# Kernel optimization log

Measured on AMD Instinct MI355X. Metric: run time of the kernel, lower is better.

## Reference

```python
import jax, jax.numpy as jnp
import numpy as np

K = 32
TEMP = 0.01
OTHERWEIGHT = 0.5
BS = 64
F = 128


def setup_inputs() -> dict:
    key = jax.random.key(0)
    k1, k2, k3 = jax.random.split(key, 3)
    feats1 = jax.random.normal(k1, (K * BS, F), dtype=jnp.float32)
    feats2 = jax.random.normal(k2, (K * BS, F), dtype=jnp.float32)
    overlap_inds = jax.random.randint(k3, (K,), 0, 2).astype(bool)
    return {"feats1": feats1, "feats2": feats2, "overlap_inds": overlap_inds, "bs": BS}


def _labels(overlap_inds, bs):
    k = overlap_inds.shape[0]
    labels1 = jnp.repeat(jnp.arange(k), bs)
    nov = (~overlap_inds).astype(jnp.int32)
    excl_nov = jnp.cumsum(nov) - nov  # exclusive count of non-overlaps before i
    class2 = jnp.where(overlap_inds, jnp.arange(k), k + excl_nov)
    labels2 = jnp.repeat(class2, bs)
    return jnp.concatenate([labels1, labels2])


def reference(feats1, feats2, overlap_inds, bs):
    n1 = feats1.shape[0]
    labels = _labels(overlap_inds, bs)            # [n]
    feats = jnp.concatenate([feats1, feats2])     # [n, F]
    n = feats.shape[0]

    logits = (feats @ feats.T) * TEMP             # [n, n]; log of exp(sim*temp)
    sim = jnp.exp(logits)

    same = labels[:, None] == labels[None, :]
    eye = jnp.eye(n, dtype=bool)
    pos_mask = same & ~eye
    neg_mask = ~same

    is2 = jnp.arange(n) >= n1                     # second-view block indicator
    cross_w = jnp.where(is2[:, None] != is2[None, :], OTHERWEIGHT, 1.0)

    neg_sum = jnp.sum(jnp.where(neg_mask, sim, 0.0), axis=1)      # [n]
    # -log(pos / neg_sum) = log(neg_sum) - logits
    per_pair_loss = cross_w * (jnp.log(neg_sum)[:, None] - logits)
    total_loss = jnp.sum(jnp.where(pos_mask, per_pair_loss, 0.0))
    total_pos = jnp.sum(pos_mask)

    # accuracy: a positive pair counts iff its sim beats ALL negatives in its row
    max_neg = jnp.max(jnp.where(neg_mask, sim, -jnp.inf), axis=1)  # [n]
    correct = pos_mask & (sim > max_neg[:, None])
    acc = jnp.sum(correct).astype(jnp.float32) / total_pos.astype(jnp.float32)

    loss = total_loss / total_pos.astype(jnp.float32)
    return acc, loss
```

## Files before the change

kernel.cpp:

```cpp
#include <hip/hip_runtime.h>
#include <math.h>

#define TEMP 0.01f

typedef __attribute__((ext_vector_type(8))) short short8;
typedef __attribute__((ext_vector_type(4))) float f32x4;
typedef __attribute__((ext_vector_type(8))) unsigned short ushort8_t;


__device__ __forceinline__ unsigned bf16_hi_bits(float x) {
  unsigned u = __float_as_uint(x);
  return (u + 0x7FFFu + ((u >> 16) & 1u)) >> 16;
}

struct HL { unsigned short h, l; };

__device__ __forceinline__ HL split1(float x) {
  unsigned hb = bf16_hi_bits(x);
  float hf = __uint_as_float(hb << 16);
  unsigned lb = bf16_hi_bits(x - hf);
  HL r;
  r.h = (unsigned short)hb;
  r.l = (unsigned short)lb;
  return r;
}

__device__ __forceinline__ void decode_ov(const int* __restrict__ ov_raw,
                                          int* s_class2, int* s_v2b,
                                          int* s_ov) {
  const int t = threadIdx.x;
  if (t < 64) {
    int v = (t < 32) ? ov_raw[t] : 0;
    bool valid = (t >= 32) || (v == 0) || (v == 1);
    unsigned long long okmask = __ballot(valid);
    bool as_int = (okmask == ~0ull);
    s_v2b[t] = 0;
    if (t < 32) {
      int o = as_int ? v : (((const unsigned char*)ov_raw)[t] ? 1 : 0);
      s_ov[t] = o;
      unsigned long long nz = __ballot((t < 32) && !o);
      int cum = __popcll(nz & ((1ull << t) - 1ull));
      int c2 = o ? t : 32 + cum;
      s_class2[t] = c2;
      s_v2b[c2] = t;
    }
  }
}

__device__ __forceinline__ int labf(int g, const int* s_class2) {
  return (g < 2048) ? (g >> 6) : s_class2[(g - 2048) >> 6];
}

__device__ __forceinline__ int slotf(int g, int cls, const int* s_v2b) {
  if (g < 2048) return g - (cls << 6);
  return ((cls < 32) ? 64 : 0) + (g - 2048 - (s_v2b[cls] << 6));
}

__global__ __launch_bounds__(256) void precompute_kernel(
    const float* __restrict__ f1, const float* __restrict__ f2,
    unsigned short* __restrict__ Ph, unsigned short* __restrict__ Pl,
    float* __restrict__ accum, int* __restrict__ counter) {
  if (blockIdx.x == 0 && threadIdx.x == 0) {
    accum[0] = 0.f; accum[1] = 0.f; accum[2] = 0.f; *counter = 0;
  }
  const int u = blockIdx.x * 256 + threadIdx.x;
  const int row = u >> 4;
  const int gid = u & 15;
  const int kc = gid >> 3, P = gid & 7;
  const int k = kc * 64 + (P ^ (row & 7)) * 8;
  const float* src = (row < 2048) ? (f1 + (size_t)row * 128)
                                  : (f2 + (size_t)(row - 2048) * 128);
  const float4 a = *(const float4*)(src + k);
  const float4 b = *(const float4*)(src + k + 4);
  ushort8_t hi, lo;
  HL s;
  s = split1(a.x); hi.s0 = s.h; lo.s0 = s.l;
  s = split1(a.y); hi.s1 = s.h; lo.s1 = s.l;
  s = split1(a.z); hi.s2 = s.h; lo.s2 = s.l;
  s = split1(a.w); hi.s3 = s.h; lo.s3 = s.l;
  s = split1(b.x); hi.s4 = s.h; lo.s4 = s.l;
  s = split1(b.y); hi.s5 = s.h; lo.s5 = s.l;
  s = split1(b.z); hi.s6 = s.h; lo.s6 = s.l;
  s = split1(b.w); hi.s7 = s.h; lo.s7 = s.l;
  *(ushort8_t*)&Ph[(size_t)row * 128 + gid * 8] = hi;
  *(ushort8_t*)&Pl[(size_t)row * 128 + gid * 8] = lo;
}

__device__ __forceinline__ void compute_tile(
    int bi, int bj, bool diag,
    const unsigned short* __restrict__ Ph, const unsigned short* __restrict__ Pl,
    unsigned short (*Ah)[64], unsigned short (*Al)[64],
    unsigned short (*Bh)[64], unsigned short (*Bl)[64],
    const int* s_class2, const int* s_v2b,
    float4* __restrict__ P4, float* __restrict__ posbuf) {
  const int ibase = bi * 128, jbase = bj * 128;
  const int t = threadIdx.x;
  const int l = t & 63;
  const int wid = t >> 6;
  const int wy = wid >> 1, wx = wid & 1;
  const int rr = l & 15;
  const int q = l >> 4;
  const int sw = l & 7;

  f32x4 acc[4][4];
#pragma unroll
  for (int mi = 0; mi < 4; ++mi)
#pragma unroll
    for (int ni = 0; ni < 4; ++ni) acc[mi][ni] = (f32x4)0.0f;

  const int gg = t & 7;
  const int r0 = t >> 3;

  for (int kc = 0; kc < 2; ++kc) {
    __syncthreads();
#pragma unroll
    for (int p = 0; p < 4; ++p) {
      const int r = r0 + 32 * p;
      const size_t arec = (size_t)(ibase + r) * 128 + kc * 64 + gg * 8;
      const ushort8_t vah = *(const ushort8_t*)&Ph[arec];
      const ushort8_t val = *(const ushort8_t*)&Pl[arec];
      *(ushort8_t*)&Ah[r][gg * 8] = vah;
      *(ushort8_t*)&Al[r][gg * 8] = val;
      if (!diag) {
        const size_t brec = (size_t)(jbase + r) * 128 + kc * 64 + gg * 8;
        const ushort8_t vbh = *(const ushort8_t*)&Ph[brec];
        const ushort8_t vbl = *(const ushort8_t*)&Pl[brec];
        *(ushort8_t*)&Bh[r][gg * 8] = vbh;
        *(ushort8_t*)&Bl[r][gg * 8] = vbl;
      }
    }
    __syncthreads();

#pragma unroll
    for (int s = 0; s < 2; ++s) {
      const int pb = ((((s << 2) | q)) ^ sw) << 3;
      short8 afh[4], afl[4], bfh[4], bfl[4];
#pragma unroll
      for (int mi = 0; mi < 4; ++mi) {
        const int ar = wy * 64 + mi * 16 + rr;
        afh[mi] = *(const short8*)&Ah[ar][pb];
        afl[mi] = *(const short8*)&Al[ar][pb];
        const int br = wx * 64 + mi * 16 + rr;
        bfh[mi] = diag ? *(const short8*)&Ah[br][pb]
                       : *(const short8*)&Bh[br][pb];
        bfl[mi] = diag ? *(const short8*)&Al[br][pb]
                       : *(const short8*)&Bl[br][pb];
      }
#pragma unroll
      for (int mi = 0; mi < 4; ++mi)
#pragma unroll
        for (int ni = 0; ni < 4; ++ni) {
          acc[mi][ni] = __builtin_amdgcn_mfma_f32_16x16x32_bf16(
              afh[mi], bfh[ni], acc[mi][ni], 0, 0, 0);
          acc[mi][ni] = __builtin_amdgcn_mfma_f32_16x16x32_bf16(
              afh[mi], bfl[ni], acc[mi][ni], 0, 0, 0);
          acc[mi][ni] = __builtin_amdgcn_mfma_f32_16x16x32_bf16(
              afl[mi], bfh[ni], acc[mi][ni], 0, 0, 0);
        }
    }
  }

  const bool off = !diag;
  const float cw = ((ibase < 2048) != (jbase < 2048)) ? 0.5f : 1.0f;

  float* RowPn = (float*)&Ah[0][0];
  float* RowPl = (float*)&Al[0][0];
  float* RowPm = (float*)&Bh[0][0];
  float* ColPn = (float*)&Bl[0][0];
  float* ColPl = ColPn + 1024;
  float* ColPm = ColPn + 2048;

  int gj[4], lj[4];
#pragma unroll
  for (int ni = 0; ni < 4; ++ni) {
    gj[ni] = jbase + wx * 64 + ni * 16 + rr;
    lj[ni] = labf(gj[ni], s_class2);
  }

  float cnsum[4], cnmax[4], clsum[4];
#pragma unroll
  for (int ni = 0; ni < 4; ++ni) {
    cnsum[ni] = 0.f; cnmax[ni] = 0.f; clsum[ni] = 0.f;
  }

  __syncthreads();

#pragma unroll
  for (int mi = 0; mi < 4; ++mi) {
#pragma unroll
    for (int reg = 0; reg < 4; ++reg) {
      const int gi = ibase + wy * 64 + mi * 16 + q * 4 + reg;
      const int li = labf(gi, s_class2);
      float rn = 0.f, rl = 0.f, rm = 0.f;
#pragma unroll
      for (int ni = 0; ni < 4; ++ni) {
        const int gjj = gj[ni];
        if (gi == gjj) continue;
        const float logit = acc[mi][ni][reg] * TEMP;
        const float e = __expf(logit);
        if (li == lj[ni]) {
          rl += logit;
          posbuf[(size_t)gi * 128 + slotf(gjj, li, s_v2b)] = e;
          if (off) {
            clsum[ni] += logit;
            posbuf[(size_t)gjj * 128 + slotf(gi, li, s_v2b)] = e;
          }
        } else {
          rn += e;
          rm = fmaxf(rm, e);
          if (off) {
            cnsum[ni] += e;
            cnmax[ni] = fmaxf(cnmax[ni], e);
          }
        }
      }
      const int widx = ((mi * 4 + reg) * 4 + wid) * 64 + l;
      RowPn[widx] = rn;
      RowPl[widx] = rl;
      RowPm[widx] = rm;
    }
  }
  if (off) {
#pragma unroll
    for (int ni = 0; ni < 4; ++ni) {
      const int widx = (ni * 4 + wid) * 64 + l;
      ColPn[widx] = cnsum[ni];
      ColPl[widx] = clsum[ni];
      ColPm[widx] = cnmax[ni];
    }
  }
  __syncthreads();

  {
    const int r = t >> 1, h = t & 1;
    const int g = (((r >> 4) & 3) * 4) + (r & 3);
    const int w2 = (r >> 6) * 2 + h;
    const int base = (g * 4 + w2) * 64 + ((r >> 2) & 3) * 16;
    const float4* pn = (const float4*)&RowPn[base];
    const float4* pl = (const float4*)&RowPl[base];
    const float4* pm = (const float4*)&RowPm[base];
    float ns = 0.f, ls = 0.f, nm = 0.f;
#pragma unroll
    for (int i = 0; i < 4; ++i) {
      const float4 a = pn[i], b = pl[i], c = pm[i];
      ns += a.x + a.y + a.z + a.w;
      ls += b.x + b.y + b.z + b.w;
      nm = fmaxf(nm, fmaxf(fmaxf(c.x, c.y), fmaxf(c.z, c.w)));
    }
    float4 v; v.x = ns; v.y = 0.f; v.z = cw * ls; v.w = nm;
    P4[(size_t)(ibase + r) * 64 + (bj * 2 + h)] = v;
  }

  if (off) {
    const int c = t >> 1, hy = t & 1;
    const int w2 = hy * 2 + (c >> 6);
    const int base = (((c >> 4) & 3) * 4 + w2) * 64 + (c & 15);
    float ns = 0.f, ls = 0.f, nm = 0.f;
#pragma unroll
    for (int q4 = 0; q4 < 4; ++q4) {
      const int idx = base + q4 * 16;
      ns += ColPn[idx];
      ls += ColPl[idx];
      nm = fmaxf(nm, ColPm[idx]);
    }
    float4 v; v.x = ns; v.y = 0.f; v.z = cw * ls; v.w = nm;
    P4[(size_t)(jbase + c) * 64 + (bi * 2 + hy)] = v;
  }
}

__global__ __launch_bounds__(256, 2) void main_kernel(
    const unsigned short* __restrict__ Ph, const unsigned short* __restrict__ Pl,
    const int* __restrict__ ov_raw, float4* __restrict__ P4,
    float* __restrict__ posbuf) {
  __shared__ unsigned short Ah[128][64], Al[128][64];
  __shared__ unsigned short Bh[128][64], Bl[128][64];
  __shared__ int s_class2[32], s_v2b[64], s_ov[32];

  decode_ov(ov_raw, s_class2, s_v2b, s_ov);

  const int bid = blockIdx.x;
  if (bid < 496) {
    int idx = bid, bi = 0;
    while (idx >= 31 - bi) { idx -= 31 - bi; ++bi; }
    const int bj = bi + 1 + idx;
    compute_tile(bi, bj, false, Ph, Pl, Ah, Al, Bh, Bl, s_class2, s_v2b, P4,
                 posbuf);
  } else {
    const int d = (bid - 496) * 2;
    compute_tile(d, d, true, Ph, Pl, Ah, Al, Bh, Bl, s_class2, s_v2b, P4,
                 posbuf);
    compute_tile(d + 1, d + 1, true, Ph, Pl, Ah, Al, Bh, Bl, s_class2, s_v2b,
                 P4, posbuf);
  }
}

__global__ __launch_bounds__(256) void finalize_kernel(
    const int* __restrict__ ov_raw, const float4* __restrict__ P4,
    const float* __restrict__ posbuf, float* __restrict__ accum,
    int* __restrict__ counter, float* __restrict__ out) {
  __shared__ int s_class2[32], s_v2b[64], s_ov[32];
  __shared__ float sc[4], sp[4], sl[4];
  decode_ov(ov_raw, s_class2, s_v2b, s_ov);
  __syncthreads();

  const int t = threadIdx.x;
  const int w = t >> 6, lane = t & 63;
  float cnt_acc = 0.f, pos_acc = 0.f, loss_acc = 0.f;
  const int rbase = blockIdx.x * 16 + w * 4;
  for (int i = 0; i < 4; ++i) {
    const int row = rbase + i;
    float4 p = P4[(size_t)row * 64 + lane];
#pragma unroll
    for (int m = 1; m < 64; m <<= 1) {
      p.x += __shfl_xor(p.x, m, 64);
      p.z += __shfl_xor(p.z, m, 64);
      p.w = fmaxf(p.w, __shfl_xor(p.w, m, 64));
    }
    const float nmax = p.w;
    const float2 pv = *(const float2*)&posbuf[(size_t)row * 128 + lane * 2];
    const int c = labf(row, s_class2);
    const bool both = (row < 2048) ? (s_ov[c] != 0) : (c < 32);
    const int size = both ? 128 : 64;
    int selfslot;
    if (row < 2048) selfslot = row - (c << 6);
    else selfslot = ((c < 32) ? 64 : 0) + (row - 2048 - (s_v2b[c] << 6));
    const int s0 = lane * 2;
    int h = 0;
    if (s0 < size && s0 != selfslot && pv.x > nmax) h++;
    if (s0 + 1 < size && s0 + 1 != selfslot && pv.y > nmax) h++;
    cnt_acc += (float)h;
    if (lane == 0) {
      const float pcw = both ? 95.f : 63.f;
      loss_acc += logf(p.x) * pcw - p.z;
      pos_acc += (float)(size - 1);
    }
  }
#pragma unroll
  for (int m = 1; m < 64; m <<= 1) {
    cnt_acc += __shfl_xor(cnt_acc, m, 64);
    pos_acc += __shfl_xor(pos_acc, m, 64);
    loss_acc += __shfl_xor(loss_acc, m, 64);
  }
  if (lane == 0) { sc[w] = cnt_acc; sp[w] = pos_acc; sl[w] = loss_acc; }
  __syncthreads();
  if (t == 0) {
    atomicAdd(&accum[0], sc[0] + sc[1] + sc[2] + sc[3]);
    atomicAdd(&accum[1], sp[0] + sp[1] + sp[2] + sp[3]);
    atomicAdd(&accum[2], sl[0] + sl[1] + sl[2] + sl[3]);
    __threadfence();
    const int prev = atomicAdd(counter, 1);
    if (prev == 255) {
      const float c = atomicAdd(&accum[0], 0.0f);
      const float tp = atomicAdd(&accum[1], 0.0f);
      const float lo = atomicAdd(&accum[2], 0.0f);
      out[0] = c / tp;
      out[1] = lo / tp;
    }
  }
}

extern "C" void kernel_launch(void* const* d_in, const int* in_sizes, int n_in,
                              void* d_out, int out_size, void* d_ws,
                              size_t ws_size, hipStream_t stream) {
  const float* f1 = (const float*)d_in[0];
  const float* f2 = (const float*)d_in[1];
  const int* ov = (const int*)d_in[2];
  float* out = (float*)d_out;

  float* wsf = (float*)d_ws;
  int* wsi = (int*)d_ws;
  float* accum  = wsf;
  int* counter  = wsi + 3;
  float* posbuf = wsf + 16;
  float4* P4    = (float4*)(wsf + 524304);
  unsigned short* Ph = (unsigned short*)(wsf + 1572880);
  unsigned short* Pl = Ph + 524288;

  precompute_kernel<<<256, 256, 0, stream>>>(f1, f2, Ph, Pl, accum, counter);
  main_kernel<<<512, 256, 0, stream>>>(Ph, Pl, ov, P4, posbuf);
  finalize_kernel<<<256, 256, 0, stream>>>(ov, P4, posbuf, accum, counter,
                                           out);
}
```

Before: 106.4 us.

## Fuse precompute, main and finalize kernels into one persistent mega kernel

Removes the separate bf16 hi/lo split pre-pass: each tile now loads fp32 features directly and splits them while staging into shared memory, at the cost of recomputing the split for every tile that reads a row. The finalize pass is folded into the main kernel. The last 128 blocks to finish, chosen by ticket order, spin-wait on a global counter until all 512 blocks are done, then reduce the partials. A memset replaces the in-kernel accumulator reset. This saves two kernel launches and the Ph/Pl global round trip, but relies on every block being co-resident or finishing before the waiters spin, which is a deadlock risk.

Result: slower. 171.0 us (+60.7%).

```diff
diff --git a/kernel.cpp b/kernel.cpp
--- a/kernel.cpp
+++ b/kernel.cpp
@@ -5,7 +5,7 @@
 
 typedef __attribute__((ext_vector_type(8))) short short8;
 typedef __attribute__((ext_vector_type(4))) float f32x4;
-typedef __attribute__((ext_vector_type(8))) unsigned short ushort8_t;
+typedef __attribute__((ext_vector_type(4))) unsigned short ushort4_t;
 
 
 __device__ __forceinline__ unsigned bf16_hi_bits(float x) {
@@ -56,44 +56,18 @@
   return ((cls < 32) ? 64 : 0) + (g - 2048 - (s_v2b[cls] << 6));
 }
 
-__global__ __launch_bounds__(256) void precompute_kernel(
-    const float* __restrict__ f1, const float* __restrict__ f2,
-    unsigned short* __restrict__ Ph, unsigned short* __restrict__ Pl,
-    float* __restrict__ accum, int* __restrict__ counter) {
-  if (blockIdx.x == 0 && threadIdx.x == 0) {
-    accum[0] = 0.f; accum[1] = 0.f; accum[2] = 0.f; *counter = 0;
-  }
-  const int u = blockIdx.x * 256 + threadIdx.x;
-  const int row = u >> 4;
-  const int gid = u & 15;
-  const int kc = gid >> 3, P = gid & 7;
-  const int k = kc * 64 + (P ^ (row & 7)) * 8;
-  const float* src = (row < 2048) ? (f1 + (size_t)row * 128)
-                                  : (f2 + (size_t)(row - 2048) * 128);
-  const float4 a = *(const float4*)(src + k);
-  const float4 b = *(const float4*)(src + k + 4);
-  ushort8_t hi, lo;
-  HL s;
-  s = split1(a.x); hi.s0 = s.h; lo.s0 = s.l;
-  s = split1(a.y); hi.s1 = s.h; lo.s1 = s.l;
-  s = split1(a.z); hi.s2 = s.h; lo.s2 = s.l;
-  s = split1(a.w); hi.s3 = s.h; lo.s3 = s.l;
-  s = split1(b.x); hi.s4 = s.h; lo.s4 = s.l;
-  s = split1(b.y); hi.s5 = s.h; lo.s5 = s.l;
-  s = split1(b.z); hi.s6 = s.h; lo.s6 = s.l;
-  s = split1(b.w); hi.s7 = s.h; lo.s7 = s.l;
-  *(ushort8_t*)&Ph[(size_t)row * 128 + gid * 8] = hi;
-  *(ushort8_t*)&Pl[(size_t)row * 128 + gid * 8] = lo;
-}
-
 __device__ __forceinline__ void compute_tile(
     int bi, int bj, bool diag,
-    const unsigned short* __restrict__ Ph, const unsigned short* __restrict__ Pl,
+    const float* __restrict__ f1, const float* __restrict__ f2,
     unsigned short (*Ah)[64], unsigned short (*Al)[64],
     unsigned short (*Bh)[64], unsigned short (*Bl)[64],
     const int* s_class2, const int* s_v2b,
     float4* __restrict__ P4, float* __restrict__ posbuf) {
   const int ibase = bi * 128, jbase = bj * 128;
+  const float* asrc = (ibase < 2048) ? (f1 + (size_t)ibase * 128)
+                                     : (f2 + (size_t)(ibase - 2048) * 128);
+  const float* bsrc = (jbase < 2048) ? (f1 + (size_t)jbase * 128)
+                                     : (f2 + (size_t)(jbase - 2048) * 128);
   const int t = threadIdx.x;
   const int l = t & 63;
   const int wid = t >> 6;
@@ -108,25 +82,33 @@
 #pragma unroll
     for (int ni = 0; ni < 4; ++ni) acc[mi][ni] = (f32x4)0.0f;
 
-  const int gg = t & 7;
-  const int r0 = t >> 3;
+  const int kq = t & 15;
+  const int r0 = t >> 4;
+  const int stc = ((kq >> 1) ^ (r0 & 7)) * 8 + (kq & 1) * 4;
 
   for (int kc = 0; kc < 2; ++kc) {
     __syncthreads();
 #pragma unroll
-    for (int p = 0; p < 4; ++p) {
-      const int r = r0 + 32 * p;
-      const size_t arec = (size_t)(ibase + r) * 128 + kc * 64 + gg * 8;
-      const ushort8_t vah = *(const ushort8_t*)&Ph[arec];
-      const ushort8_t val = *(const ushort8_t*)&Pl[arec];
-      *(ushort8_t*)&Ah[r][gg * 8] = vah;
-      *(ushort8_t*)&Al[r][gg * 8] = val;
+    for (int p = 0; p < 8; ++p) {
+      const int r = r0 + 16 * p;
+      const float4 va = *(const float4*)(asrc + (size_t)r * 128 + kc * 64 + kq * 4);
+      ushort4_t ha, la;
+      HL s;
+      s = split1(va.x); ha.x = s.h; la.x = s.l;
+      s = split1(va.y); ha.y = s.h; la.y = s.l;
+      s = split1(va.z); ha.z = s.h; la.z = s.l;
+      s = split1(va.w); ha.w = s.h; la.w = s.l;
+      *(ushort4_t*)&Ah[r][stc] = ha;
+      *(ushort4_t*)&Al[r][stc] = la;
       if (!diag) {
-        const size_t brec = (size_t)(jbase + r) * 128 + kc * 64 + gg * 8;
-        const ushort8_t vbh = *(const ushort8_t*)&Ph[brec];
-        const ushort8_t vbl = *(const ushort8_t*)&Pl[brec];
-        *(ushort8_t*)&Bh[r][gg * 8] = vbh;
-        *(ushort8_t*)&Bl[r][gg * 8] = vbl;
+        const float4 vb = *(const float4*)(bsrc + (size_t)r * 128 + kc * 64 + kq * 4);
+        ushort4_t hb, lb;
+        s = split1(vb.x); hb.x = s.h; lb.x = s.l;
+        s = split1(vb.y); hb.y = s.h; lb.y = s.l;
+        s = split1(vb.z); hb.z = s.h; lb.z = s.l;
+        s = split1(vb.w); hb.w = s.h; lb.w = s.l;
+        *(ushort4_t*)&Bh[r][stc] = hb;
+        *(ushort4_t*)&Bl[r][stc] = lb;
       }
     }
     __syncthreads();
@@ -268,13 +250,17 @@
   }
 }
 
-__global__ __launch_bounds__(256, 2) void main_kernel(
-    const unsigned short* __restrict__ Ph, const unsigned short* __restrict__ Pl,
+__global__ __launch_bounds__(256, 2) void mega_kernel(
+    const float* __restrict__ f1, const float* __restrict__ f2,
     const int* __restrict__ ov_raw, float4* __restrict__ P4,
-    float* __restrict__ posbuf) {
+    float* __restrict__ posbuf, float* __restrict__ accum,
+    int* __restrict__ counter, int* __restrict__ counter2,
+    float* __restrict__ out) {
   __shared__ unsigned short Ah[128][64], Al[128][64];
   __shared__ unsigned short Bh[128][64], Bl[128][64];
   __shared__ int s_class2[32], s_v2b[64], s_ov[32];
+  __shared__ int s_ticket;
+  __shared__ float sc[4], sp[4], sl[4];
 
   decode_ov(ov_raw, s_class2, s_v2b, s_ov);
 
@@ -283,31 +269,34 @@
     int idx = bid, bi = 0;
     while (idx >= 31 - bi) { idx -= 31 - bi; ++bi; }
     const int bj = bi + 1 + idx;
-    compute_tile(bi, bj, false, Ph, Pl, Ah, Al, Bh, Bl, s_class2, s_v2b, P4,
+    compute_tile(bi, bj, false, f1, f2, Ah, Al, Bh, Bl, s_class2, s_v2b, P4,
                  posbuf);
   } else {
     const int d = (bid - 496) * 2;
-    compute_tile(d, d, true, Ph, Pl, Ah, Al, Bh, Bl, s_class2, s_v2b, P4,
+    compute_tile(d, d, true, f1, f2, Ah, Al, Bh, Bl, s_class2, s_v2b, P4,
                  posbuf);
-    compute_tile(d + 1, d + 1, true, Ph, Pl, Ah, Al, Bh, Bl, s_class2, s_v2b,
+    compute_tile(d + 1, d + 1, true, f1, f2, Ah, Al, Bh, Bl, s_class2, s_v2b,
                  P4, posbuf);
   }
-}
-
-__global__ __launch_bounds__(256) void finalize_kernel(
-    const int* __restrict__ ov_raw, const float4* __restrict__ P4,
-    const float* __restrict__ posbuf, float* __restrict__ accum,
-    int* __restrict__ counter, float* __restrict__ out) {
-  __shared__ int s_class2[32], s_v2b[64], s_ov[32];
-  __shared__ float sc[4], sp[4], sl[4];
-  decode_ov(ov_raw, s_class2, s_v2b, s_ov);
-  __syncthreads();
-
+
+  __threadfence();
   const int t = threadIdx.x;
+  if (t == 0) s_ticket = atomicAdd(counter, 1);
+  __syncthreads();
+  const int ticket = s_ticket;
+  if (ticket < 384) return;
+
+  if (t == 0) {
+    while (atomicAdd(counter, 0) < 512) __builtin_amdgcn_s_sleep(2);
+  }
+  __syncthreads();
+  __threadfence();
+
+  const int slice = ticket - 384;
   const int w = t >> 6, lane = t & 63;
   float cnt_acc = 0.f, pos_acc = 0.f, loss_acc = 0.f;
-  const int rbase = blockIdx.x * 16 + w * 4;
-  for (int i = 0; i < 4; ++i) {
+  const int rbase = slice * 32 + w * 8;
+  for (int i = 0; i < 8; ++i) {
     const int row = rbase + i;
     float4 p = P4[(size_t)row * 64 + lane];
 #pragma unroll
@@ -348,8 +337,8 @@
     atomicAdd(&accum[1], sp[0] + sp[1] + sp[2] + sp[3]);
     atomicAdd(&accum[2], sl[0] + sl[1] + sl[2] + sl[3]);
     __threadfence();
-    const int prev = atomicAdd(counter, 1);
-    if (prev == 255) {
+    const int tk2 = atomicAdd(counter2, 1);
+    if (tk2 == 127) {
       const float c = atomicAdd(&accum[0], 0.0f);
       const float tp = atomicAdd(&accum[1], 0.0f);
       const float lo = atomicAdd(&accum[2], 0.0f);
@@ -371,13 +360,12 @@
   int* wsi = (int*)d_ws;
   float* accum  = wsf;
   int* counter  = wsi + 3;
+  int* counter2 = wsi + 4;
   float* posbuf = wsf + 16;
   float4* P4    = (float4*)(wsf + 524304);
-  unsigned short* Ph = (unsigned short*)(wsf + 1572880);
-  unsigned short* Pl = Ph + 524288;
-
-  precompute_kernel<<<256, 256, 0, stream>>>(f1, f2, Ph, Pl, accum, counter);
-  main_kernel<<<512, 256, 0, stream>>>(Ph, Pl, ov, P4, posbuf);
-  finalize_kernel<<<256, 256, 0, stream>>>(ov, P4, posbuf, accum, counter,
-                                           out);
-}
+
+  (void)hipMemsetAsync(accum, 0, 32, stream);
+
+  mega_kernel<<<512, 256, 0, stream>>>(f1, f2, ov, P4, posbuf, accum, counter,
+                                       counter2, out);
+}
```
